# Optimization experiments

Measured on AMD Instinct MI355X. Metric: run time of the kernel, lower is better.

Reference implementation:

```python
import jax, jax.numpy as jnp
import numpy as np

T = 2048      # num_tokens == max_seq_len
D = 4096      # d_in
H = 32        # num_heads
G = 8         # num_kv_groups
HD = 128      # head_dim
GS = H // G   # group_size = 4
EPS = 1e-6


def _make_rope(t, hd):
    inv_freq = 1.0 / (10000.0 ** (np.arange(0, hd, 2, dtype=np.float64) / hd))
    freqs = np.outer(np.arange(t, dtype=np.float64), inv_freq)      # [T, HD/2]
    emb = np.concatenate([freqs, freqs], axis=-1)                   # [T, HD]
    return (jnp.asarray(np.cos(emb), jnp.float32),
            jnp.asarray(np.sin(emb), jnp.float32))


def setup_inputs() -> dict:
    key = jax.random.key(0)
    ks = jax.random.split(key, 6)
    x = jax.random.normal(ks[0], (T, D), jnp.float32)
    # causal mask: True = masked (upper triangle above diagonal)
    mask = jnp.triu(jnp.ones((T, T), jnp.bool_), k=1)
    cos, sin = _make_rope(T, HD)
    s = 0.02
    Wq = jax.random.normal(ks[1], (D, H * HD), jnp.float32) * s
    Wk = jax.random.normal(ks[2], (D, G * HD), jnp.float32) * s
    Wv = jax.random.normal(ks[3], (D, G * HD), jnp.float32) * s
    Wo = jax.random.normal(ks[4], (H * HD, D), jnp.float32) * s
    qn_w = jnp.ones((HD,), jnp.float32)
    kn_w = jnp.ones((HD,), jnp.float32)
    return {"x": x, "mask": mask, "cos": cos, "sin": sin,
            "Wq": Wq, "Wk": Wk, "Wv": Wv, "Wo": Wo,
            "qn_w": qn_w, "kn_w": kn_w}


def _rmsnorm(u, w):
    # normalize over head_dim (last axis), eps inside sqrt
    var = jnp.mean(jnp.square(u), axis=-1, keepdims=True)
    return u * jax.lax.rsqrt(var + EPS) * w


def _rope(u, cos, sin):
    # rotate-half RoPE; u: [heads, T, HD], cos/sin: [T, HD]
    hd = u.shape[-1]
    u1, u2 = u[..., : hd // 2], u[..., hd // 2:]
    rot = jnp.concatenate([-u2, u1], axis=-1)
    return u * cos[None] + rot * sin[None]


def reference(x, mask, cos, sin, Wq, Wk, Wv, Wo, qn_w, kn_w):
    t = x.shape[0]
    q = (x @ Wq).reshape(t, H, HD).transpose(1, 0, 2)   # [H, T, HD]
    k = (x @ Wk).reshape(t, G, HD).transpose(1, 0, 2)   # [G, T, HD]
    v = (x @ Wv).reshape(t, G, HD).transpose(1, 0, 2)   # [G, T, HD]
    q = _rmsnorm(q, qn_w)
    k = _rmsnorm(k, kn_w)
    q = _rope(q, cos, sin)
    k = _rope(k, cos, sin)
    # GQA expansion: repeat_interleave along head axis
    k = jnp.repeat(k, GS, axis=0)                       # [H, T, HD]
    v = jnp.repeat(v, GS, axis=0)                       # [H, T, HD]
    scores = jnp.einsum('hqd,hkd->hqk', q, k) / (HD ** 0.5)
    scores = jnp.where(mask[None], -jnp.inf, scores)
    w = jax.nn.softmax(scores, axis=-1)
    attn = jnp.einsum('hqk,hkd->hqd', w, v)             # [H, T, HD]
    attn = attn.transpose(1, 0, 2).reshape(t, H * HD)
    return attn @ Wo
```

## Files before the change

kernel.cpp:

```cpp
#include <hip/hip_runtime.h>

#define T_ 2048
#define D_ 4096
#define H_ 32
#define G_ 8
#define HD_ 128

typedef float f32x4 __attribute__((ext_vector_type(4)));
typedef __bf16 bf16x8 __attribute__((ext_vector_type(8)));
typedef unsigned short u16x8 __attribute__((ext_vector_type(8)));
typedef unsigned short u16x4 __attribute__((ext_vector_type(4)));

__device__ __forceinline__ unsigned short f2bf(float f) {
  unsigned u = __builtin_bit_cast(unsigned, f);
  u += 0x7FFFu + ((u >> 16) & 1u);
  return (unsigned short)(u >> 16);
}
__device__ __forceinline__ float bf2f(unsigned short h) {
  return __builtin_bit_cast(float, (unsigned)h << 16);
}

__device__ __forceinline__ void gload_lds16(const unsigned short* g, unsigned short* l) {
  __builtin_amdgcn_global_load_lds((const __attribute__((address_space(1))) void*)g,
                                   (__attribute__((address_space(3))) void*)l, 16, 0, 0);
}

__global__ __launch_bounds__(256) void convert_bf16(const float* __restrict__ in,
                                                    unsigned short* __restrict__ out) {
  const size_t i = ((size_t)blockIdx.x * 256 + threadIdx.x) * 8;
  float4 a = *(const float4*)(in + i);
  float4 b = *(const float4*)(in + i + 4);
  u16x8 o;
  o[0] = f2bf(a.x); o[1] = f2bf(a.y); o[2] = f2bf(a.z); o[3] = f2bf(a.w);
  o[4] = f2bf(b.x); o[5] = f2bf(b.y); o[6] = f2bf(b.z); o[7] = f2bf(b.w);
  *(u16x8*)(out + i) = o;
}

__global__ __launch_bounds__(256) void transpose_convert(const float* __restrict__ Wm,
                                                         unsigned short* __restrict__ Wt,
                                                         int R, int C) {
  __shared__ float tile[64][65];
  const int r0 = blockIdx.x * 64, c0 = blockIdx.y * 64;
  const int lr4 = threadIdx.x >> 6, lc = threadIdx.x & 63;
#pragma unroll
  for (int i = 0; i < 16; ++i) {
    int r = i * 4 + lr4;
    tile[r][lc] = Wm[(size_t)(r0 + r) * C + c0 + lc];
  }
  __syncthreads();
#pragma unroll
  for (int i = 0; i < 16; ++i) {
    int r = i * 4 + lr4;
    Wt[(size_t)(c0 + r) * R + r0 + lc] = f2bf(tile[lc][r]);
  }
}

__global__ __launch_bounds__(256) void transpose_v(const unsigned short* __restrict__ v,
                                                   unsigned short* __restrict__ vt, int stride) {
  __shared__ unsigned short tile[64][65];
  const int t0 = blockIdx.x * 64, d0 = blockIdx.y * 64, g = blockIdx.z;
  const int lr4 = threadIdx.x >> 6, lc = threadIdx.x & 63;
#pragma unroll
  for (int i = 0; i < 16; ++i) {
    int r = i * 4 + lr4;
    tile[r][lc] = v[(size_t)(t0 + r) * stride + g * HD_ + d0 + lc];
  }
  __syncthreads();
#pragma unroll
  for (int i = 0; i < 16; ++i) {
    int r = i * 4 + lr4;
    vt[((size_t)g * HD_ + d0 + r) * T_ + t0 + lc] = tile[lc][r];
  }
}

__global__ __launch_bounds__(256) void norm_rope(const unsigned short* __restrict__ raw,
                                                 int stride,
                                                 unsigned short* __restrict__ outp,
                                                 const float* __restrict__ w,
                                                 const float* __restrict__ cs,
                                                 const float* __restrict__ sn, int NH) {
  const int row = blockIdx.x * 4 + (threadIdx.x >> 6);
  const int lane = threadIdx.x & 63;
  const int t = row / NH, h = row - t * NH;
  const unsigned short* src = raw + (size_t)t * stride + h * HD_;
  float u1 = bf2f(src[lane]);
  float u2 = bf2f(src[lane + 64]);
  float ss = u1 * u1 + u2 * u2;
#pragma unroll
  for (int m = 1; m < 64; m <<= 1) ss += __shfl_xor(ss, m);
  float rr = rsqrtf(ss * (1.f / 128.f) + 1e-6f);
  float c = cs[(size_t)t * HD_ + lane];
  float s = sn[(size_t)t * HD_ + lane];
  float a = u1 * rr * w[lane];
  float b = u2 * rr * w[lane + 64];
  unsigned short* dst = outp + ((size_t)h * T_ + t) * HD_;
  dst[lane]      = f2bf(a * c - b * s);
  dst[lane + 64] = f2bf(b * c + a * s);
}

template <int NF, int F0, int F1>
__device__ __forceinline__ void mfma_g(f32x4 (&acc)[4][NF], bf16x8 (&af)[4][2],
                                       bf16x8 (&bf)[NF][2]) {
  __builtin_amdgcn_s_setprio(1);
#pragma unroll
  for (int fm = 0; fm < 4; ++fm)
#pragma unroll
    for (int fn = F0; fn < F1; ++fn) {
      f32x4 a = acc[fm][fn];
      a = __builtin_amdgcn_mfma_f32_16x16x32_bf16(af[fm][0], bf[fn][0], a, 0, 0, 0);
      a = __builtin_amdgcn_mfma_f32_16x16x32_bf16(af[fm][1], bf[fn][1], a, 0, 0, 0);
      acc[fm][fn] = a;
    }
  __builtin_amdgcn_s_setprio(0);
}

template <int NF, int OUTF32>
__global__ __launch_bounds__(512, 4) void gemm3(const unsigned short* __restrict__ A,
                                                const unsigned short* __restrict__ Bt,
                                                void* __restrict__ Cv, int M, int N,
                                                int K, int LDA) {
  constexpr int BN = NF * 64;
  constexpr int BBUF = NF * 4096;
  __shared__ __align__(16) unsigned short lds[16384 + 2 * BBUF];
  const int tid = threadIdx.x;
  const int wid = tid >> 6, lane = tid & 63;
  const int lr = lane & 15, lhi = lane >> 4;
  const int wr = wid >> 2, wcn = wid & 3;

  int flat = blockIdx.y * gridDim.x + blockIdx.x;
  int nwg = gridDim.x * gridDim.y;
  int swz = (flat & 7) * (nwg >> 3) + (flat >> 3);
  const int brow = (swz & 15) * 128;
  const int bcol = (swz >> 4) * BN;

  const int nt = K >> 6;

  f32x4 acc[4][NF];
#pragma unroll
  for (int b = 0; b < 4; ++b)
#pragma unroll
    for (int c = 0; c < NF; ++c) acc[b][c] = (f32x4){0.f, 0.f, 0.f, 0.f};

  const int t8 = tid >> 3;
  const int srcCol = ((tid & 7) ^ (t8 & 7)) * 8;
  auto stageA = [&](int d, int u, int ktp) {
    gload_lds16(A + (size_t)(brow + u * 64 + t8) * LDA + ktp * 64 + srcCol,
                &lds[d * 8192 + u * 4096 + tid * 8]);
  };
  auto stageB = [&](int d, int v, int ktp) {
    gload_lds16(Bt + (size_t)(bcol + v * 64 + t8) * LDA + ktp * 64 + srcCol,
                &lds[16384 + d * BBUF + v * 4096 + tid * 8]);
  };

  bf16x8 af[4][2], bf[NF][2];
  auto readA = [&](int d) {
#pragma unroll
    for (int fm = 0; fm < 4; ++fm) {
      int row = wr * 64 + fm * 16 + lr;
      int base = d * 8192 + row * 64;
      int sw = (row & 7) << 3;
      af[fm][0] = *(const bf16x8*)&lds[base + ((lhi * 8) ^ sw)];
      af[fm][1] = *(const bf16x8*)&lds[base + ((32 + lhi * 8) ^ sw)];
    }
  };
  auto readBf = [&](int d, int fn, bf16x8 (&slot)[2]) {
    int row = wcn * (16 * NF) + fn * 16 + lr;
    int base = 16384 + d * BBUF + row * 64;
    int sw = (row & 7) << 3;
    slot[0] = *(const bf16x8*)&lds[base + ((lhi * 8) ^ sw)];
    slot[1] = *(const bf16x8*)&lds[base + ((32 + lhi * 8) ^ sw)];
  };

  stageA(0, 0, 0); stageA(0, 1, 0);
#pragma unroll
  for (int v = 0; v < NF; ++v) stageB(0, v, 0);
  stageA(1, 0, 1); stageA(1, 1, 1);
  asm volatile("s_waitcnt vmcnt(2)" ::: "memory");
  __builtin_amdgcn_s_barrier();

  for (int t = 0; t < nt; ++t) {
    const int d = t & 1, dn = d ^ 1;
    if constexpr (NF == 3) {
      readA(d); readBf(d, 0, bf[0]); readBf(d, 1, bf[1]);
      if (t + 1 < nt) { stageB(dn, 0, t + 1); stageB(dn, 1, t + 1); stageB(dn, 2, t + 1); }
      __builtin_amdgcn_s_barrier();
      mfma_g<NF, 0, 2>(acc, af, bf);
      __builtin_amdgcn_s_barrier();
      readBf(d, 2, bf[2]);
      if (t + 2 < nt) { stageA(d, 0, t + 2); stageA(d, 1, t + 2); }
      __builtin_amdgcn_s_barrier();
      mfma_g<NF, 2, 3>(acc, af, bf);
      if (t < nt - 2) asm volatile("s_waitcnt vmcnt(2)" ::: "memory");
      else if (t == nt - 2) asm volatile("s_waitcnt vmcnt(0)" ::: "memory");
      __builtin_amdgcn_s_barrier();
    } else {
      readA(d); readBf(d, 0, bf[0]);
      if (t + 1 < nt) { stageB(dn, 0, t + 1); stageB(dn, 1, t + 1); }
      __builtin_amdgcn_s_barrier();
      mfma_g<NF, 0, 1>(acc, af, bf);
      __builtin_amdgcn_s_barrier();
      readBf(d, 1, bf[1]);
      if (t + 2 < nt) { stageA(d, 0, t + 2); stageA(d, 1, t + 2); }
      __builtin_amdgcn_s_barrier();
      mfma_g<NF, 1, 2>(acc, af, bf);
      if (t < nt - 2) asm volatile("s_waitcnt vmcnt(2)" ::: "memory");
      else if (t == nt - 2) asm volatile("s_waitcnt vmcnt(0)" ::: "memory");
      __builtin_amdgcn_s_barrier();
    }
  }

#pragma unroll
  for (int fm = 0; fm < 4; ++fm)
#pragma unroll
    for (int fn = 0; fn < NF; ++fn) {
      int col = bcol + wcn * (16 * NF) + fn * 16 + lr;
#pragma unroll
      for (int r = 0; r < 4; ++r) {
        int row = brow + wr * 64 + fm * 16 + lhi * 4 + r;
        if (OUTF32)
          ((float*)Cv)[(size_t)row * N + col] = acc[fm][fn][r];
        else
          ((unsigned short*)Cv)[(size_t)row * N + col] = f2bf(acc[fm][fn][r]);
      }
    }
}

__global__ __launch_bounds__(512) void flash_attn(const unsigned short* __restrict__ q,
                                                  const unsigned short* __restrict__ k,
                                                  const unsigned short* __restrict__ vt,
                                                  unsigned short* __restrict__ attnb) {
  const int pairIdx = blockIdx.y;
  const int g = pairIdx >> 1;
  const int qcp = blockIdx.x;
  const int tid = threadIdx.x;
  const int wid = tid >> 6;
  const int lane = tid & 63;
  const int lr = lane & 15, lhi = lane >> 4;
  const int h = pairIdx * 2 + (wid >> 2);

  __shared__ __align__(16) unsigned short Ks[2][64 * HD_];
  __shared__ __align__(16) unsigned short Vs[2][HD_ * 64];
  __shared__ __align__(16) unsigned short p_lds_all[8][16 * 64];
  unsigned short* p_lds = p_lds_all[wid];

  const unsigned short* kg = k + (size_t)g * T_ * HD_;
  const unsigned short* vg = vt + (size_t)g * HD_ * T_;

  int ko[2], vo[2];
#pragma unroll
  for (int p = 0; p < 2; ++p) {
    int ob = (p * 512 + tid) * 16;
    int krow = ob >> 8, kb = ob & 255;
    ko[p] = krow * HD_ + ((kb ^ ((krow & 7) << 4)) >> 1);
    int vrow = ob >> 7, vb2 = ob & 127;
    vo[p] = vrow * T_ + ((vb2 ^ ((vrow & 7) << 4)) >> 1);
  }
  const int lbase = wid * 512;

  const int sx = (lr & 7) << 4;
  const float scale2 = 0.08838834764831845f * 1.4426950408889634f;

  for (int pass = 0; pass < 2; ++pass) {
    const int qc = pass ? (31 - qcp) : qcp;
    const int q0 = qc * 64 + (wid & 3) * 16;

    bf16x8 qf[4];
    {
      const unsigned short* qrow = q + ((size_t)h * T_ + q0 + lr) * HD_ + lhi * 8;
#pragma unroll
      for (int c = 0; c < 4; ++c) qf[c] = *(const bf16x8*)(qrow + c * 32);
    }
    f32x4 accO[8];
#pragma unroll
    for (int i = 0; i < 8; ++i) accO[i] = (f32x4){0.f, 0.f, 0.f, 0.f};
    float mrow = -3e38f;
    float lrow = 0.f;

    const int ntile = qc + 1;

#pragma unroll
    for (int p = 0; p < 2; ++p) {
      gload_lds16(kg + ko[p], &Ks[0][p * 4096 + lbase]);
      gload_lds16(vg + vo[p], &Vs[0][p * 4096 + lbase]);
    }
    __syncthreads();

    for (int kt = 0; kt < ntile; ++kt) {
      const int b = kt & 1;
      const int kv0 = kt << 6;
      if (kt + 1 < ntile) {
        const size_t kofs = (size_t)(kv0 + 64) * HD_;
#pragma unroll
        for (int p = 0; p < 2; ++p) {
          gload_lds16(kg + kofs + ko[p], &Ks[b ^ 1][p * 4096 + lbase]);
          gload_lds16(vg + (kv0 + 64) + vo[p], &Vs[b ^ 1][p * 4096 + lbase]);
        }
      }
      f32x4 st[4];
      __builtin_amdgcn_s_setprio(1);
#pragma unroll
      for (int j = 0; j < 4; ++j) {
        st[j] = (f32x4){0.f, 0.f, 0.f, 0.f};
        const int krow = j * 16 + lr;
#pragma unroll
        for (int c = 0; c < 4; ++c) {
          bf16x8 kf = *(const bf16x8*)&Ks[b][krow * HD_ + (((c * 64 + lhi * 16) ^ sx) >> 1)];
          st[j] = __builtin_amdgcn_mfma_f32_16x16x32_bf16(kf, qf[c], st[j], 0, 0, 0);
        }
      }
      __builtin_amdgcn_s_setprio(0);
      if (kt == ntile - 1) {
#pragma unroll
        for (int j = 0; j < 4; ++j)
#pragma unroll
          for (int r = 0; r < 4; ++r)
            st[j][r] = (kv0 + j * 16 + lhi * 4 + r <= q0 + lr) ? st[j][r] * scale2 : -3e38f;
      } else {
#pragma unroll
        for (int j = 0; j < 4; ++j)
#pragma unroll
          for (int r = 0; r < 4; ++r) st[j][r] *= scale2;
      }
      float pm = st[0][0];
#pragma unroll
      for (int j = 0; j < 4; ++j)
#pragma unroll
        for (int r = 0; r < 4; ++r) pm = fmaxf(pm, st[j][r]);
      pm = fmaxf(pm, __shfl_xor(pm, 16));
      pm = fmaxf(pm, __shfl_xor(pm, 32));
      if (!__all(pm - mrow <= 8.f)) {
        float mnew = fmaxf(mrow, pm);
        float al = __builtin_amdgcn_exp2f(mrow - mnew);
        mrow = mnew;
        lrow *= al;
        float a0 = __shfl(al, lhi * 4 + 0);
        float a1 = __shfl(al, lhi * 4 + 1);
        float a2 = __shfl(al, lhi * 4 + 2);
        float a3 = __shfl(al, lhi * 4 + 3);
#pragma unroll
        for (int dt = 0; dt < 8; ++dt) {
          accO[dt][0] *= a0; accO[dt][1] *= a1; accO[dt][2] *= a2; accO[dt][3] *= a3;
        }
      }
      float ps = 0.f;
#pragma unroll
      for (int j = 0; j < 4; ++j)
#pragma unroll
        for (int r = 0; r < 4; ++r) {
          float e = __builtin_amdgcn_exp2f(st[j][r] - mrow);
          st[j][r] = e;
          ps += e;
        }
      ps += __shfl_xor(ps, 16);
      ps += __shfl_xor(ps, 32);
      lrow += ps;
#pragma unroll
      for (int j = 0; j < 4; ++j) {
        u16x4 pw;
        pw[0] = f2bf(st[j][0]); pw[1] = f2bf(st[j][1]);
        pw[2] = f2bf(st[j][2]); pw[3] = f2bf(st[j][3]);
        *(u16x4*)&p_lds[lr * 64 + (((j * 32 + lhi * 8) ^ sx) >> 1)] = pw;
      }
      bf16x8 pa0 = *(const bf16x8*)&p_lds[lr * 64 + (((lhi * 16) ^ sx) >> 1)];
      bf16x8 pa1 = *(const bf16x8*)&p_lds[lr * 64 + (((64 + lhi * 16) ^ sx) >> 1)];
      __builtin_amdgcn_s_setprio(1);
#pragma unroll
      for (int dt = 0; dt < 8; ++dt) {
        const int vrow = dt * 16 + lr;
        bf16x8 vf0 = *(const bf16x8*)&Vs[b][vrow * 64 + (((lhi * 16) ^ sx) >> 1)];
        bf16x8 vf1 = *(const bf16x8*)&Vs[b][vrow * 64 + (((64 + lhi * 16) ^ sx) >> 1)];
        accO[dt] = __builtin_amdgcn_mfma_f32_16x16x32_bf16(pa0, vf0, accO[dt], 0, 0, 0);
        accO[dt] = __builtin_amdgcn_mfma_f32_16x16x32_bf16(pa1, vf1, accO[dt], 0, 0, 0);
      }
      __builtin_amdgcn_s_setprio(0);
      __syncthreads();
    }
    float rinv = 1.f / lrow;
    float i0 = __shfl(rinv, lhi * 4 + 0);
    float i1 = __shfl(rinv, lhi * 4 + 1);
    float i2 = __shfl(rinv, lhi * 4 + 2);
    float i3 = __shfl(rinv, lhi * 4 + 3);
    float iv[4] = {i0, i1, i2, i3};
#pragma unroll
    for (int r = 0; r < 4; ++r) {
      size_t rowoff = (size_t)(q0 + lhi * 4 + r) * (H_ * HD_) + h * HD_;
#pragma unroll
      for (int dt = 0; dt < 8; ++dt) attnb[rowoff + dt * 16 + lr] = f2bf(accO[dt][r] * iv[r]);
    }
  }
}

extern "C" void kernel_launch(void* const* d_in, const int* in_sizes, int n_in,
                              void* d_out, int out_size, void* d_ws, size_t ws_size,
                              hipStream_t stream) {
  const float* x = (const float*)d_in[0];
  const float* cosT = (const float*)d_in[2];
  const float* sinT = (const float*)d_in[3];
  const float* Wq = (const float*)d_in[4];
  const float* Wk = (const float*)d_in[5];
  const float* Wv = (const float*)d_in[6];
  const float* Wo = (const float*)d_in[7];
  const float* qn = (const float*)d_in[8];
  const float* kn = (const float*)d_in[9];

  unsigned char* w = (unsigned char*)d_ws;
  unsigned short* xb     = (unsigned short*)(w);
  unsigned short* WqkvT  = (unsigned short*)(w + 16777216);
  unsigned short* qkvraw = (unsigned short*)(w + 67108864);
  unsigned short* qbuf   = (unsigned short*)(w + 92274688);
  unsigned short* kbuf   = (unsigned short*)(w + 109051904);
  unsigned short* vtb    = (unsigned short*)(w + 113246208);
  unsigned short* WoT    = WqkvT;
  unsigned short* attnb  = xb;

  convert_bf16<<<dim3(4096), dim3(256), 0, stream>>>(x, xb);
  transpose_convert<<<dim3(64, 64), dim3(256), 0, stream>>>(Wq, WqkvT, 4096, 4096);
  transpose_convert<<<dim3(64, 16), dim3(256), 0, stream>>>(Wk, WqkvT + (size_t)4096 * 4096, 4096, 1024);
  transpose_convert<<<dim3(64, 16), dim3(256), 0, stream>>>(Wv, WqkvT + (size_t)5120 * 4096, 4096, 1024);

  gemm3<3, 0><<<dim3(16, 32), dim3(512), 0, stream>>>(xb, WqkvT, (void*)qkvraw, 2048, 6144, 4096, 4096);

  norm_rope<<<dim3(16384), dim3(256), 0, stream>>>(qkvraw, 6144, qbuf, qn, cosT, sinT, H_);
  norm_rope<<<dim3(4096), dim3(256), 0, stream>>>(qkvraw + 4096, 6144, kbuf, kn, cosT, sinT, G_);
  transpose_v<<<dim3(32, 2, 8), dim3(256), 0, stream>>>(qkvraw + 5120, vtb, 6144);
  transpose_convert<<<dim3(64, 64), dim3(256), 0, stream>>>(Wo, WoT, 4096, 4096);

  flash_attn<<<dim3(16, 16), dim3(512), 0, stream>>>(qbuf, kbuf, vtb, attnb);

  gemm3<2, 1><<<dim3(16, 32), dim3(512), 0, stream>>>(attnb, WoT, d_out, 2048, 4096, 4096, 4096);
}
```

Measured before the change: 342.0 us.

## Process two heads per wave in flash attention to reuse K/V fragment loads

Flash attention blocks shrink from 8 to 4 waves. Each wave now computes 16 query rows for both heads of its pair, so every K and V fragment read from LDS feeds two MFMAs instead of one. This halves LDS fragment traffic per unit of MFMA work and halves the number of threads that share the tile loads. In exchange, register pressure roughly doubles (two accumulator sets and two softmax states), which can lower occupancy, and there are fewer waves per block to hide latency.

```diff
diff --git a/kernel.cpp b/kernel.cpp
--- a/kernel.cpp
+++ b/kernel.cpp
@@ -225,31 +225,29 @@
     }
 }
 
-__global__ __launch_bounds__(512) void flash_attn(const unsigned short* __restrict__ q,
+__global__ __launch_bounds__(256) void flash_attn(const unsigned short* __restrict__ q,
                                                   const unsigned short* __restrict__ k,
                                                   const unsigned short* __restrict__ vt,
                                                   unsigned short* __restrict__ attnb) {
-  const int pairIdx = blockIdx.y;
-  const int g = pairIdx >> 1;
+  const int hp = blockIdx.y;
+  const int g = hp >> 1;
+  const int h0 = hp * 2;
   const int qcp = blockIdx.x;
   const int tid = threadIdx.x;
   const int wid = tid >> 6;
   const int lane = tid & 63;
   const int lr = lane & 15, lhi = lane >> 4;
-  const int h = pairIdx * 2 + (wid >> 2);
 
   __shared__ __align__(16) unsigned short Ks[2][64 * HD_];
   __shared__ __align__(16) unsigned short Vs[2][HD_ * 64];
-  __shared__ __align__(16) unsigned short p_lds_all[8][16 * 64];
-  unsigned short* p_lds = p_lds_all[wid];
-
+  __shared__ __align__(16) unsigned short p_lds_all[4][2][16 * 64];
   const unsigned short* kg = k + (size_t)g * T_ * HD_;
   const unsigned short* vg = vt + (size_t)g * HD_ * T_;
 
-  int ko[2], vo[2];
-#pragma unroll
-  for (int p = 0; p < 2; ++p) {
-    int ob = (p * 512 + tid) * 16;
+  int ko[4], vo[4];
+#pragma unroll
+  for (int p = 0; p < 4; ++p) {
+    int ob = (p * 256 + tid) * 16;
     int krow = ob >> 8, kb = ob & 255;
     ko[p] = krow * HD_ + ((kb ^ ((krow & 7) << 4)) >> 1);
     int vrow = ob >> 7, vb2 = ob & 127;
@@ -262,26 +260,29 @@
 
   for (int pass = 0; pass < 2; ++pass) {
     const int qc = pass ? (31 - qcp) : qcp;
-    const int q0 = qc * 64 + (wid & 3) * 16;
-
-    bf16x8 qf[4];
+    const int q0 = qc * 64 + wid * 16;
+
+    bf16x8 qf0[4], qf1[4];
     {
-      const unsigned short* qrow = q + ((size_t)h * T_ + q0 + lr) * HD_ + lhi * 8;
-#pragma unroll
-      for (int c = 0; c < 4; ++c) qf[c] = *(const bf16x8*)(qrow + c * 32);
-    }
-    f32x4 accO[8];
-#pragma unroll
-    for (int i = 0; i < 8; ++i) accO[i] = (f32x4){0.f, 0.f, 0.f, 0.f};
-    float mrow = -3e38f;
-    float lrow = 0.f;
+      const unsigned short* qr0 = q + ((size_t)h0 * T_ + q0 + lr) * HD_ + lhi * 8;
+      const unsigned short* qr1 = qr0 + (size_t)T_ * HD_;
+#pragma unroll
+      for (int c = 0; c < 4; ++c) { qf0[c] = *(const bf16x8*)(qr0 + c * 32);
+                                    qf1[c] = *(const bf16x8*)(qr1 + c * 32); }
+    }
+    f32x4 accO0[8], accO1[8];
+#pragma unroll
+    for (int i = 0; i < 8; ++i) { accO0[i] = (f32x4){0.f, 0.f, 0.f, 0.f};
+                                  accO1[i] = (f32x4){0.f, 0.f, 0.f, 0.f}; }
+    float mrow0 = -3e38f, mrow1 = -3e38f;
+    float lrow0 = 0.f, lrow1 = 0.f;
 
     const int ntile = qc + 1;
 
 #pragma unroll
-    for (int p = 0; p < 2; ++p) {
-      gload_lds16(kg + ko[p], &Ks[0][p * 4096 + lbase]);
-      gload_lds16(vg + vo[p], &Vs[0][p * 4096 + lbase]);
+    for (int p = 0; p < 4; ++p) {
+      gload_lds16(kg + ko[p], &Ks[0][p * 2048 + lbase]);
+      gload_lds16(vg + vo[p], &Vs[0][p * 2048 + lbase]);
     }
     __syncthreads();
 
@@ -291,21 +292,23 @@
       if (kt + 1 < ntile) {
         const size_t kofs = (size_t)(kv0 + 64) * HD_;
 #pragma unroll
-        for (int p = 0; p < 2; ++p) {
-          gload_lds16(kg + kofs + ko[p], &Ks[b ^ 1][p * 4096 + lbase]);
-          gload_lds16(vg + (kv0 + 64) + vo[p], &Vs[b ^ 1][p * 4096 + lbase]);
+        for (int p = 0; p < 4; ++p) {
+          gload_lds16(kg + kofs + ko[p], &Ks[b ^ 1][p * 2048 + lbase]);
+          gload_lds16(vg + (kv0 + 64) + vo[p], &Vs[b ^ 1][p * 2048 + lbase]);
         }
       }
-      f32x4 st[4];
+      f32x4 st0[4], st1[4];
       __builtin_amdgcn_s_setprio(1);
 #pragma unroll
       for (int j = 0; j < 4; ++j) {
-        st[j] = (f32x4){0.f, 0.f, 0.f, 0.f};
+        st0[j] = (f32x4){0.f, 0.f, 0.f, 0.f};
+        st1[j] = (f32x4){0.f, 0.f, 0.f, 0.f};
         const int krow = j * 16 + lr;
 #pragma unroll
         for (int c = 0; c < 4; ++c) {
           bf16x8 kf = *(const bf16x8*)&Ks[b][krow * HD_ + (((c * 64 + lhi * 16) ^ sx) >> 1)];
-          st[j] = __builtin_amdgcn_mfma_f32_16x16x32_bf16(kf, qf[c], st[j], 0, 0, 0);
+          st0[j] = __builtin_amdgcn_mfma_f32_16x16x32_bf16(kf, qf0[c], st0[j], 0, 0, 0);
+          st1[j] = __builtin_amdgcn_mfma_f32_16x16x32_bf16(kf, qf1[c], st1[j], 0, 0, 0);
         }
       }
       __builtin_amdgcn_s_setprio(0);
@@ -313,79 +316,113 @@
 #pragma unroll
         for (int j = 0; j < 4; ++j)
 #pragma unroll
-          for (int r = 0; r < 4; ++r)
-            st[j][r] = (kv0 + j * 16 + lhi * 4 + r <= q0 + lr) ? st[j][r] * scale2 : -3e38f;
+          for (int r = 0; r < 4; ++r) {
+            bool ok = kv0 + j * 16 + lhi * 4 + r <= q0 + lr;
+            st0[j][r] = ok ? st0[j][r] * scale2 : -3e38f;
+            st1[j][r] = ok ? st1[j][r] * scale2 : -3e38f;
+          }
       } else {
 #pragma unroll
         for (int j = 0; j < 4; ++j)
 #pragma unroll
-          for (int r = 0; r < 4; ++r) st[j][r] *= scale2;
-      }
-      float pm = st[0][0];
+          for (int r = 0; r < 4; ++r) { st0[j][r] *= scale2; st1[j][r] *= scale2; }
+      }
+      float pm0 = st0[0][0], pm1 = st1[0][0];
 #pragma unroll
       for (int j = 0; j < 4; ++j)
 #pragma unroll
-        for (int r = 0; r < 4; ++r) pm = fmaxf(pm, st[j][r]);
-      pm = fmaxf(pm, __shfl_xor(pm, 16));
-      pm = fmaxf(pm, __shfl_xor(pm, 32));
-      if (!__all(pm - mrow <= 8.f)) {
-        float mnew = fmaxf(mrow, pm);
-        float al = __builtin_amdgcn_exp2f(mrow - mnew);
-        mrow = mnew;
-        lrow *= al;
-        float a0 = __shfl(al, lhi * 4 + 0);
-        float a1 = __shfl(al, lhi * 4 + 1);
-        float a2 = __shfl(al, lhi * 4 + 2);
-        float a3 = __shfl(al, lhi * 4 + 3);
+        for (int r = 0; r < 4; ++r) { pm0 = fmaxf(pm0, st0[j][r]); pm1 = fmaxf(pm1, st1[j][r]); }
+      pm0 = fmaxf(pm0, __shfl_xor(pm0, 16)); pm0 = fmaxf(pm0, __shfl_xor(pm0, 32));
+      pm1 = fmaxf(pm1, __shfl_xor(pm1, 16)); pm1 = fmaxf(pm1, __shfl_xor(pm1, 32));
+      if (!__all(pm0 - mrow0 <= 8.f)) {
+        float mnew = fmaxf(mrow0, pm0);
+        float al = __builtin_amdgcn_exp2f(mrow0 - mnew);
+        mrow0 = mnew; lrow0 *= al;
+        float a0 = __shfl(al, lhi * 4 + 0), a1 = __shfl(al, lhi * 4 + 1);
+        float a2 = __shfl(al, lhi * 4 + 2), a3 = __shfl(al, lhi * 4 + 3);
 #pragma unroll
         for (int dt = 0; dt < 8; ++dt) {
-          accO[dt][0] *= a0; accO[dt][1] *= a1; accO[dt][2] *= a2; accO[dt][3] *= a3;
+          accO0[dt][0] *= a0; accO0[dt][1] *= a1; accO0[dt][2] *= a2; accO0[dt][3] *= a3;
         }
       }
-      float ps = 0.f;
+      if (!__all(pm1 - mrow1 <= 8.f)) {
+        float mnew = fmaxf(mrow1, pm1);
+        float al = __builtin_amdgcn_exp2f(mrow1 - mnew);
+        mrow1 = mnew; lrow1 *= al;
+        float a0 = __shfl(al, lhi * 4 + 0), a1 = __shfl(al, lhi * 4 + 1);
+        float a2 = __shfl(al, lhi * 4 + 2), a3 = __shfl(al, lhi * 4 + 3);
+#pragma unroll
+        for (int dt = 0; dt < 8; ++dt) {
+          accO1[dt][0] *= a0; accO1[dt][1] *= a1; accO1[dt][2] *= a2; accO1[dt][3] *= a3;
+        }
+      }
+      float ps0 = 0.f, ps1 = 0.f;
 #pragma unroll
       for (int j = 0; j < 4; ++j)
 #pragma unroll
         for (int r = 0; r < 4; ++r) {
-          float e = __builtin_amdgcn_exp2f(st[j][r] - mrow);
-          st[j][r] = e;
-          ps += e;
+          float e0 = __builtin_amdgcn_exp2f(st0[j][r] - mrow0);
+          float e1 = __builtin_amdgcn_exp2f(st1[j][r] - mrow1);
+          st0[j][r] = e0; st1[j][r] = e1;
+          ps0 += e0; ps1 += e1;
         }
-      ps += __shfl_xor(ps, 16);
-      ps += __shfl_xor(ps, 32);
-      lrow += ps;
+      ps0 += __shfl_xor(ps0, 16); ps0 += __shfl_xor(ps0, 32);
+      ps1 += __shfl_xor(ps1, 16); ps1 += __shfl_xor(ps1, 32);
+      lrow0 += ps0; lrow1 += ps1;
+      unsigned short* p0 = p_lds_all[wid][0];
+      unsigned short* p1 = p_lds_all[wid][1];
 #pragma unroll
       for (int j = 0; j < 4; ++j) {
-        u16x4 pw;
-        pw[0] = f2bf(st[j][0]); pw[1] = f2bf(st[j][1]);
-        pw[2] = f2bf(st[j][2]); pw[3] = f2bf(st[j][3]);
-        *(u16x4*)&p_lds[lr * 64 + (((j * 32 + lhi * 8) ^ sx) >> 1)] = pw;
-      }
-      bf16x8 pa0 = *(const bf16x8*)&p_lds[lr * 64 + (((lhi * 16) ^ sx) >> 1)];
-      bf16x8 pa1 = *(const bf16x8*)&p_lds[lr * 64 + (((64 + lhi * 16) ^ sx) >> 1)];
+        u16x4 pw0, pw1;
+        pw0[0] = f2bf(st0[j][0]); pw0[1] = f2bf(st0[j][1]);
+        pw0[2] = f2bf(st0[j][2]); pw0[3] = f2bf(st0[j][3]);
+        pw1[0] = f2bf(st1[j][0]); pw1[1] = f2bf(st1[j][1]);
+        pw1[2] = f2bf(st1[j][2]); pw1[3] = f2bf(st1[j][3]);
+        int off = lr * 64 + (((j * 32 + lhi * 8) ^ sx) >> 1);
+        *(u16x4*)&p0[off] = pw0;
+        *(u16x4*)&p1[off] = pw1;
+      }
+      int ra = lr * 64 + (((lhi * 16) ^ sx) >> 1);
+      int rb = lr * 64 + (((64 + lhi * 16) ^ sx) >> 1);
+      bf16x8 pa00 = *(const bf16x8*)&p0[ra], pa01 = *(const bf16x8*)&p0[rb];
+      bf16x8 pa10 = *(const bf16x8*)&p1[ra], pa11 = *(const bf16x8*)&p1[rb];
       __builtin_amdgcn_s_setprio(1);
 #pragma unroll
       for (int dt = 0; dt < 8; ++dt) {
         const int vrow = dt * 16 + lr;
         bf16x8 vf0 = *(const bf16x8*)&Vs[b][vrow * 64 + (((lhi * 16) ^ sx) >> 1)];
         bf16x8 vf1 = *(const bf16x8*)&Vs[b][vrow * 64 + (((64 + lhi * 16) ^ sx) >> 1)];
-        accO[dt] = __builtin_amdgcn_mfma_f32_16x16x32_bf16(pa0, vf0, accO[dt], 0, 0, 0);
-        accO[dt] = __builtin_amdgcn_mfma_f32_16x16x32_bf16(pa1, vf1, accO[dt], 0, 0, 0);
+        accO0[dt] = __builtin_amdgcn_mfma_f32_16x16x32_bf16(pa00, vf0, accO0[dt], 0, 0, 0);
+        accO0[dt] = __builtin_amdgcn_mfma_f32_16x16x32_bf16(pa01, vf1, accO0[dt], 0, 0, 0);
+        accO1[dt] = __builtin_amdgcn_mfma_f32_16x16x32_bf16(pa10, vf0, accO1[dt], 0, 0, 0);
+        accO1[dt] = __builtin_amdgcn_mfma_f32_16x16x32_bf16(pa11, vf1, accO1[dt], 0, 0, 0);
       }
       __builtin_amdgcn_s_setprio(0);
       __syncthreads();
     }
-    float rinv = 1.f / lrow;
-    float i0 = __shfl(rinv, lhi * 4 + 0);
-    float i1 = __shfl(rinv, lhi * 4 + 1);
-    float i2 = __shfl(rinv, lhi * 4 + 2);
-    float i3 = __shfl(rinv, lhi * 4 + 3);
-    float iv[4] = {i0, i1, i2, i3};
-#pragma unroll
-    for (int r = 0; r < 4; ++r) {
-      size_t rowoff = (size_t)(q0 + lhi * 4 + r) * (H_ * HD_) + h * HD_;
-#pragma unroll
-      for (int dt = 0; dt < 8; ++dt) attnb[rowoff + dt * 16 + lr] = f2bf(accO[dt][r] * iv[r]);
+    {
+      float rinv = 1.f / lrow0;
+      float i0 = __shfl(rinv, lhi * 4 + 0), i1 = __shfl(rinv, lhi * 4 + 1);
+      float i2 = __shfl(rinv, lhi * 4 + 2), i3 = __shfl(rinv, lhi * 4 + 3);
+      float iv[4] = {i0, i1, i2, i3};
+#pragma unroll
+      for (int r = 0; r < 4; ++r) {
+        size_t rowoff = (size_t)(q0 + lhi * 4 + r) * (H_ * HD_) + h0 * HD_;
+#pragma unroll
+        for (int dt = 0; dt < 8; ++dt) attnb[rowoff + dt * 16 + lr] = f2bf(accO0[dt][r] * iv[r]);
+      }
+    }
+    {
+      float rinv = 1.f / lrow1;
+      float i0 = __shfl(rinv, lhi * 4 + 0), i1 = __shfl(rinv, lhi * 4 + 1);
+      float i2 = __shfl(rinv, lhi * 4 + 2), i3 = __shfl(rinv, lhi * 4 + 3);
+      float iv[4] = {i0, i1, i2, i3};
+#pragma unroll
+      for (int r = 0; r < 4; ++r) {
+        size_t rowoff = (size_t)(q0 + lhi * 4 + r) * (H_ * HD_) + (h0 + 1) * HD_;
+#pragma unroll
+        for (int dt = 0; dt < 8; ++dt) attnb[rowoff + dt * 16 + lr] = f2bf(accO1[dt][r] * iv[r]);
+      }
     }
   }
 }
@@ -425,7 +462,7 @@
   transpose_v<<<dim3(32, 2, 8), dim3(256), 0, stream>>>(qkvraw + 5120, vtb, 6144);
   transpose_convert<<<dim3(64, 64), dim3(256), 0, stream>>>(Wo, WoT, 4096, 4096);
 
-  flash_attn<<<dim3(16, 16), dim3(512), 0, stream>>>(qbuf, kbuf, vtb, attnb);
+  flash_attn<<<dim3(16, 16), dim3(256), 0, stream>>>(qbuf, kbuf, vtb, attnb);
 
   gemm3<2, 1><<<dim3(16, 32), dim3(512), 0, stream>>>(attnb, WoT, d_out, 2048, 4096, 4096, 4096);
 }
```

After: 351.1 us. 2.7% more time.

## Restructure GEMMs to 4-wave blocks with larger per-wave output tiles

Applied to the files above, without the earlier changes.

Replaces the 8-wave 512-thread GEMM with a 4-wave 256-thread version. Each wave now computes twice as many output columns (NFW fragments), split into two halves that are loaded and multiplied in turn, while the block tile size stays the same. Each thread issues twice as many global-to-LDS loads and the vmcnt waits are adjusted to match. The aim is more MFMA work per LDS fragment read and fewer waves contending at barriers, at the cost of more accumulator registers and lower occupancy (launch bounds 256,2).

```diff
diff --git a/kernel.cpp b/kernel.cpp
--- a/kernel.cpp
+++ b/kernel.cpp
@@ -98,34 +98,36 @@
   dst[lane + 64] = f2bf(b * c + a * s);
 }
 
-template <int NF, int F0, int F1>
-__device__ __forceinline__ void mfma_g(f32x4 (&acc)[4][NF], bf16x8 (&af)[4][2],
-                                       bf16x8 (&bf)[NF][2]) {
+template <int NFW, int HALF>
+__device__ __forceinline__ void mfma_h(f32x4 (&acc)[4][NFW], bf16x8 (&af)[4][2],
+                                       bf16x8 (&bf)[NFW / 2][2]) {
   __builtin_amdgcn_s_setprio(1);
 #pragma unroll
   for (int fm = 0; fm < 4; ++fm)
 #pragma unroll
-    for (int fn = F0; fn < F1; ++fn) {
-      f32x4 a = acc[fm][fn];
-      a = __builtin_amdgcn_mfma_f32_16x16x32_bf16(af[fm][0], bf[fn][0], a, 0, 0, 0);
-      a = __builtin_amdgcn_mfma_f32_16x16x32_bf16(af[fm][1], bf[fn][1], a, 0, 0, 0);
-      acc[fm][fn] = a;
+    for (int j = 0; j < NFW / 2; ++j) {
+      constexpr int base = HALF * (NFW / 2);
+      f32x4 a = acc[fm][base + j];
+      a = __builtin_amdgcn_mfma_f32_16x16x32_bf16(af[fm][0], bf[j][0], a, 0, 0, 0);
+      a = __builtin_amdgcn_mfma_f32_16x16x32_bf16(af[fm][1], bf[j][1], a, 0, 0, 0);
+      acc[fm][base + j] = a;
     }
   __builtin_amdgcn_s_setprio(0);
 }
 
-template <int NF, int OUTF32>
-__global__ __launch_bounds__(512, 4) void gemm3(const unsigned short* __restrict__ A,
+template <int NFW, int OUTF32>
+__global__ __launch_bounds__(256, 2) void gemm4(const unsigned short* __restrict__ A,
                                                 const unsigned short* __restrict__ Bt,
                                                 void* __restrict__ Cv, int M, int N,
                                                 int K, int LDA) {
-  constexpr int BN = NF * 64;
-  constexpr int BBUF = NF * 4096;
-  __shared__ __align__(16) unsigned short lds[16384 + 2 * BBUF];
+  constexpr int BN = 32 * NFW;
+  constexpr int ABUF = 8192;
+  constexpr int BBUF = BN * 64;
+  __shared__ __align__(16) unsigned short lds[2 * ABUF + 2 * BBUF];
   const int tid = threadIdx.x;
   const int wid = tid >> 6, lane = tid & 63;
   const int lr = lane & 15, lhi = lane >> 4;
-  const int wr = wid >> 2, wcn = wid & 3;
+  const int wr = wid >> 1, wcn = wid & 1;
 
   int flat = blockIdx.y * gridDim.x + blockIdx.x;
   int nwg = gridDim.x * gridDim.y;
@@ -135,37 +137,41 @@
 
   const int nt = K >> 6;
 
-  f32x4 acc[4][NF];
+  f32x4 acc[4][NFW];
 #pragma unroll
   for (int b = 0; b < 4; ++b)
 #pragma unroll
-    for (int c = 0; c < NF; ++c) acc[b][c] = (f32x4){0.f, 0.f, 0.f, 0.f};
+    for (int c = 0; c < NFW; ++c) acc[b][c] = (f32x4){0.f, 0.f, 0.f, 0.f};
 
   const int t8 = tid >> 3;
   const int srcCol = ((tid & 7) ^ (t8 & 7)) * 8;
   auto stageA = [&](int d, int u, int ktp) {
-    gload_lds16(A + (size_t)(brow + u * 64 + t8) * LDA + ktp * 64 + srcCol,
-                &lds[d * 8192 + u * 4096 + tid * 8]);
+#pragma unroll
+    for (int l = 0; l < 2; ++l)
+      gload_lds16(A + (size_t)(brow + u * 64 + l * 32 + t8) * LDA + ktp * 64 + srcCol,
+                  &lds[d * ABUF + u * 4096 + l * 2048 + tid * 8]);
   };
   auto stageB = [&](int d, int v, int ktp) {
-    gload_lds16(Bt + (size_t)(bcol + v * 64 + t8) * LDA + ktp * 64 + srcCol,
-                &lds[16384 + d * BBUF + v * 4096 + tid * 8]);
+#pragma unroll
+    for (int l = 0; l < 2; ++l)
+      gload_lds16(Bt + (size_t)(bcol + v * 64 + l * 32 + t8) * LDA + ktp * 64 + srcCol,
+                  &lds[2 * ABUF + d * BBUF + v * 4096 + l * 2048 + tid * 8]);
   };
 
-  bf16x8 af[4][2], bf[NF][2];
+  bf16x8 af[4][2], bf[NFW / 2][2];
   auto readA = [&](int d) {
 #pragma unroll
     for (int fm = 0; fm < 4; ++fm) {
       int row = wr * 64 + fm * 16 + lr;
-      int base = d * 8192 + row * 64;
+      int base = d * ABUF + row * 64;
       int sw = (row & 7) << 3;
       af[fm][0] = *(const bf16x8*)&lds[base + ((lhi * 8) ^ sw)];
       af[fm][1] = *(const bf16x8*)&lds[base + ((32 + lhi * 8) ^ sw)];
     }
   };
   auto readBf = [&](int d, int fn, bf16x8 (&slot)[2]) {
-    int row = wcn * (16 * NF) + fn * 16 + lr;
-    int base = 16384 + d * BBUF + row * 64;
+    int row = wcn * (16 * NFW) + fn * 16 + lr;
+    int base = 2 * ABUF + d * BBUF + row * 64;
     int sw = (row & 7) << 3;
     slot[0] = *(const bf16x8*)&lds[base + ((lhi * 8) ^ sw)];
     slot[1] = *(const bf16x8*)&lds[base + ((32 + lhi * 8) ^ sw)];
@@ -173,47 +179,38 @@
 
   stageA(0, 0, 0); stageA(0, 1, 0);
 #pragma unroll
-  for (int v = 0; v < NF; ++v) stageB(0, v, 0);
+  for (int v = 0; v < NFW / 2; ++v) stageB(0, v, 0);
   stageA(1, 0, 1); stageA(1, 1, 1);
-  asm volatile("s_waitcnt vmcnt(2)" ::: "memory");
+  asm volatile("s_waitcnt vmcnt(4)" ::: "memory");
   __builtin_amdgcn_s_barrier();
 
   for (int t = 0; t < nt; ++t) {
     const int d = t & 1, dn = d ^ 1;
-    if constexpr (NF == 3) {
-      readA(d); readBf(d, 0, bf[0]); readBf(d, 1, bf[1]);
-      if (t + 1 < nt) { stageB(dn, 0, t + 1); stageB(dn, 1, t + 1); stageB(dn, 2, t + 1); }
-      __builtin_amdgcn_s_barrier();
-      mfma_g<NF, 0, 2>(acc, af, bf);
-      __builtin_amdgcn_s_barrier();
-      readBf(d, 2, bf[2]);
-      if (t + 2 < nt) { stageA(d, 0, t + 2); stageA(d, 1, t + 2); }
-      __builtin_amdgcn_s_barrier();
-      mfma_g<NF, 2, 3>(acc, af, bf);
-      if (t < nt - 2) asm volatile("s_waitcnt vmcnt(2)" ::: "memory");
-      else if (t == nt - 2) asm volatile("s_waitcnt vmcnt(0)" ::: "memory");
-      __builtin_amdgcn_s_barrier();
-    } else {
-      readA(d); readBf(d, 0, bf[0]);
-      if (t + 1 < nt) { stageB(dn, 0, t + 1); stageB(dn, 1, t + 1); }
-      __builtin_amdgcn_s_barrier();
-      mfma_g<NF, 0, 1>(acc, af, bf);
-      __builtin_amdgcn_s_barrier();
-      readBf(d, 1, bf[1]);
-      if (t + 2 < nt) { stageA(d, 0, t + 2); stageA(d, 1, t + 2); }
-      __builtin_amdgcn_s_barrier();
-      mfma_g<NF, 1, 2>(acc, af, bf);
-      if (t < nt - 2) asm volatile("s_waitcnt vmcnt(2)" ::: "memory");
-      else if (t == nt - 2) asm volatile("s_waitcnt vmcnt(0)" ::: "memory");
-      __builtin_amdgcn_s_barrier();
-    }
+    readA(d);
+#pragma unroll
+    for (int j = 0; j < NFW / 2; ++j) readBf(d, j, bf[j]);
+    if (t + 1 < nt) {
+#pragma unroll
+      for (int v = 0; v < NFW / 2; ++v) stageB(dn, v, t + 1);
+    }
+    __builtin_amdgcn_s_barrier();
+    mfma_h<NFW, 0>(acc, af, bf);
+    __builtin_amdgcn_s_barrier();
+#pragma unroll
+    for (int j = 0; j < NFW / 2; ++j) readBf(d, NFW / 2 + j, bf[j]);
+    if (t + 2 < nt) { stageA(d, 0, t + 2); stageA(d, 1, t + 2); }
+    __builtin_amdgcn_s_barrier();
+    mfma_h<NFW, 1>(acc, af, bf);
+    if (t < nt - 2) asm volatile("s_waitcnt vmcnt(4)" ::: "memory");
+    else if (t == nt - 2) asm volatile("s_waitcnt vmcnt(0)" ::: "memory");
+    __builtin_amdgcn_s_barrier();
   }
 
 #pragma unroll
   for (int fm = 0; fm < 4; ++fm)
 #pragma unroll
-    for (int fn = 0; fn < NF; ++fn) {
-      int col = bcol + wcn * (16 * NF) + fn * 16 + lr;
+    for (int fn = 0; fn < NFW; ++fn) {
+      int col = bcol + wcn * (16 * NFW) + fn * 16 + lr;
 #pragma unroll
       for (int r = 0; r < 4; ++r) {
         int row = brow + wr * 64 + fm * 16 + lhi * 4 + r;
@@ -418,7 +415,7 @@
   transpose_convert<<<dim3(64, 16), dim3(256), 0, stream>>>(Wk, WqkvT + (size_t)4096 * 4096, 4096, 1024);
   transpose_convert<<<dim3(64, 16), dim3(256), 0, stream>>>(Wv, WqkvT + (size_t)5120 * 4096, 4096, 1024);
 
-  gemm3<3, 0><<<dim3(16, 32), dim3(512), 0, stream>>>(xb, WqkvT, (void*)qkvraw, 2048, 6144, 4096, 4096);
+  gemm4<6, 0><<<dim3(16, 32), dim3(256), 0, stream>>>(xb, WqkvT, (void*)qkvraw, 2048, 6144, 4096, 4096);
 
   norm_rope<<<dim3(16384), dim3(256), 0, stream>>>(qkvraw, 6144, qbuf, qn, cosT, sinT, H_);
   norm_rope<<<dim3(4096), dim3(256), 0, stream>>>(qkvraw + 4096, 6144, kbuf, kn, cosT, sinT, G_);
@@ -427,5 +424,5 @@
 
   flash_attn<<<dim3(16, 16), dim3(512), 0, stream>>>(qbuf, kbuf, vtb, attnb);
 
-  gemm3<2, 1><<<dim3(16, 32), dim3(512), 0, stream>>>(attnb, WoT, d_out, 2048, 4096, 4096, 4096);
-}
+  gemm4<4, 1><<<dim3(16, 32), dim3(256), 0, stream>>>(attnb, WoT, d_out, 2048, 4096, 4096, 4096);
+}
```

New measurement: 325.9 us. 4.7% less time.
